# Kernel tuning notes

Hardware: AMD Instinct MI355X
Metric: run time of the kernel (lower is better)

Reference implementation:

```python
import jax, jax.numpy as jnp
import numpy as np

EPS = 1e-5
NHEAD = 8
TOP_K = 2


def _layernorm(x, g, b):
    m = jnp.mean(x, axis=-1, keepdims=True)
    v = jnp.mean((x - m) ** 2, axis=-1, keepdims=True)
    return (x - m) * jax.lax.rsqrt(v + EPS) * g + b


def setup_inputs() -> dict:
    S, D, F, E = 4096, 512, 2048, 8
    key = jax.random.key(0)
    ks = jax.random.split(key, 18)
    std = 0.02
    return {
        "src": jax.random.normal(ks[0], (S, D), jnp.float32),
        "in_proj_w": std * jax.random.normal(ks[1], (3 * D, D), jnp.float32),
        "in_proj_b": jnp.zeros((3 * D,), jnp.float32),
        "out_proj_w": std * jax.random.normal(ks[2], (D, D), jnp.float32),
        "out_proj_b": jnp.zeros((D,), jnp.float32),
        "ln1_g": jnp.ones((D,), jnp.float32),
        "ln1_b": jnp.zeros((D,), jnp.float32),
        "ln2_g": jnp.ones((D,), jnp.float32),
        "ln2_b": jnp.zeros((D,), jnp.float32),
        "gate_w": std * jax.random.normal(ks[3], (E, D), jnp.float32),
        "gate_b": jnp.zeros((E,), jnp.float32),
        "w1": std * jax.random.normal(ks[4], (E, F, D), jnp.float32),
        "b1": jnp.zeros((E, F), jnp.float32),
        "w2": std * jax.random.normal(ks[5], (E, F, D), jnp.float32),
        "b2": jnp.zeros((E, F), jnp.float32),
        "wo": std * jax.random.normal(ks[6], (E, D, F), jnp.float32),
        "bo": jnp.zeros((E, D), jnp.float32),
    }


def _sa_block(x, in_proj_w, in_proj_b, out_proj_w, out_proj_b):
    # x: [S, D] unbatched sequence (torch MultiheadAttention unbatched path)
    S, D = x.shape
    hd = D // NHEAD
    qkv = x @ in_proj_w.T + in_proj_b              # [S, 3D]
    q, k, v = jnp.split(qkv, 3, axis=-1)
    q = q.reshape(S, NHEAD, hd)
    k = k.reshape(S, NHEAD, hd)
    v = v.reshape(S, NHEAD, hd)
    scores = jnp.einsum("shd,thd->hst", q, k) / jnp.sqrt(jnp.float32(hd))
    attn = jax.nn.softmax(scores, axis=-1)         # [H, S, S]
    out = jnp.einsum("hst,thd->shd", attn, v).reshape(S, D)
    return out @ out_proj_w.T + out_proj_b


def _ff_block(x, gate_w, gate_b, w1, b1, w2, b2, wo, bo):
    # top-k gated SwiGLU MoE; gate probs are softmax, NOT renormalized after topk
    T = x.shape[0]
    E = w1.shape[0]
    gates = jax.nn.softmax(x @ gate_w.T + gate_b, axis=-1)      # [T, E]
    top_scores, top_idx = jax.lax.top_k(gates, TOP_K)            # [T, k]
    combine = jnp.zeros((T, E), x.dtype).at[
        jnp.arange(T)[:, None], top_idx].add(top_scores)         # [T, E]
    out = jnp.zeros_like(x)
    for e in range(E):  # small fixed expert count
        h = jax.nn.silu(x @ w1[e].T + b1[e]) * (x @ w2[e].T + b2[e])
        out = out + combine[:, e:e + 1] * (h @ wo[e].T + bo[e])
    return out


def reference(src, in_proj_w, in_proj_b, out_proj_w, out_proj_b,
              ln1_g, ln1_b, ln2_g, ln2_b,
              gate_w, gate_b, w1, b1, w2, b2, wo, bo):
    # norm_first pre-norm residual layer, dropout=0 (eval)
    x = src
    x = x + _sa_block(_layernorm(x, ln1_g, ln1_b),
                      in_proj_w, in_proj_b, out_proj_w, out_proj_b)
    x = x + _ff_block(_layernorm(x, ln2_g, ln2_b),
                      gate_w, gate_b, w1, b1, w2, b2, wo, bo)
    return x
```

## Files before the change

kernel.cpp:

```cpp
#include <hip/hip_runtime.h>
#include <hip/hip_bf16.h>
#include <math.h>

#define SQ   4096
#define DM   512
#define NH   8
#define HDIM 64
#define FF   2048
#define NE   8

typedef unsigned short u16;
typedef unsigned int   u32;
typedef __attribute__((ext_vector_type(8))) __bf16 bf16x8;
typedef __attribute__((ext_vector_type(4))) float  f32x4;

__device__ __forceinline__ float bf2f(u16 v) {
    union { u32 i; float f; } c; c.i = ((u32)v) << 16; return c.f;
}
__device__ __forceinline__ u16 f2bf(float f) {
    union { __bf16 h; u16 u; } c; c.h = (__bf16)f; return c.u;
}

#define BM 128
#define BN 128
#define BK 32
#define BKP 40

__global__ __launch_bounds__(256) void gemm_split(
    const u16* __restrict__ Ahi, const u16* __restrict__ Alo, int lda,
    const u16* __restrict__ Bhi, const u16* __restrict__ Blo, int ldb,
    int M, int N, int K,
    const float* __restrict__ bias,
    const float* __restrict__ resid, int ldres,
    u16* __restrict__ Chi, u16* __restrict__ Clo,
    float* __restrict__ Cf, int ldc, int mode)
{
    __shared__ __align__(16) u16 Ash[BM * BKP], Asl[BM * BKP];
    __shared__ __align__(16) u16 Bsh[BN * BKP], Bsl[BN * BKP];
    const int tid  = threadIdx.x;
    const int wave = tid >> 6;
    const int lane = tid & 63;
    const int quad = lane >> 4;
    const int l16  = lane & 15;
    const int bm = blockIdx.x * BM;
    const int bn = blockIdx.y * BN;
    const int wm = (wave & 1) * 64;
    const int wn = (wave >> 1) * 64;

    f32x4 acc[4][4];
#pragma unroll
    for (int i = 0; i < 4; i++)
#pragma unroll
        for (int j = 0; j < 4; j++)
#pragma unroll
            for (int r = 0; r < 4; r++) acc[i][j][r] = 0.0f;

    for (int k0 = 0; k0 < K; k0 += BK) {
#pragma unroll
        for (int i = 0; i < 2; i++) {
            int c = tid + i * 256;
            int row = c >> 2;
            int col = (c & 3) << 3;
            int ga = bm + row, gb2 = bn + row;
            uint4 vah = make_uint4(0u,0u,0u,0u), val = vah, vbh = vah, vbl = vah;
            if (ga < M) {
                vah = *(const uint4*)(Ahi + (size_t)ga * lda + k0 + col);
                val = *(const uint4*)(Alo + (size_t)ga * lda + k0 + col);
            }
            if (gb2 < N) {
                vbh = *(const uint4*)(Bhi + (size_t)gb2 * ldb + k0 + col);
                vbl = *(const uint4*)(Blo + (size_t)gb2 * ldb + k0 + col);
            }
            *(uint4*)(Ash + row * BKP + col) = vah;
            *(uint4*)(Asl + row * BKP + col) = val;
            *(uint4*)(Bsh + row * BKP + col) = vbh;
            *(uint4*)(Bsl + row * BKP + col) = vbl;
        }
        __syncthreads();
        bf16x8 ah[4], al[4], bh[4], bl[4];
#pragma unroll
        for (int i = 0; i < 4; i++) {
            ah[i] = *(const bf16x8*)(Ash + (wm + i * 16 + l16) * BKP + quad * 8);
            al[i] = *(const bf16x8*)(Asl + (wm + i * 16 + l16) * BKP + quad * 8);
        }
#pragma unroll
        for (int j = 0; j < 4; j++) {
            bh[j] = *(const bf16x8*)(Bsh + (wn + j * 16 + l16) * BKP + quad * 8);
            bl[j] = *(const bf16x8*)(Bsl + (wn + j * 16 + l16) * BKP + quad * 8);
        }
#pragma unroll
        for (int i = 0; i < 4; i++)
#pragma unroll
            for (int j = 0; j < 4; j++) {
                acc[i][j] = __builtin_amdgcn_mfma_f32_16x16x32_bf16(ah[i], bh[j], acc[i][j], 0,0,0);
                acc[i][j] = __builtin_amdgcn_mfma_f32_16x16x32_bf16(ah[i], bl[j], acc[i][j], 0,0,0);
                acc[i][j] = __builtin_amdgcn_mfma_f32_16x16x32_bf16(al[i], bh[j], acc[i][j], 0,0,0);
            }
        __syncthreads();
    }

#pragma unroll
    for (int i = 0; i < 4; i++)
#pragma unroll
        for (int j = 0; j < 4; j++)
#pragma unroll
            for (int r = 0; r < 4; r++) {
                int row = bm + wm + i * 16 + quad * 4 + r;
                int col = bn + wn + j * 16 + l16;
                if (row >= M || col >= N) continue;
                float v = acc[i][j][r] + (bias ? bias[col] : 0.0f);
                size_t idx = (size_t)row * ldc + col;
                if (mode == 0) {
                    u16 hb = f2bf(v);
                    Chi[idx] = hb;
                    Clo[idx] = f2bf(v - bf2f(hb));
                } else {
                    if (resid) v += resid[(size_t)row * ldres + col];
                    Cf[idx] = v;
                }
            }
}

__global__ __launch_bounds__(256) void gemm_split_ko(
    const u16* __restrict__ Ahi, const u16* __restrict__ Alo, int lda,
    const u16* __restrict__ Bhi, const u16* __restrict__ Blo, int ldb,
    float* __restrict__ Cf, int ldc)
{
    __shared__ __align__(16) u16 Ash[BM * BKP], Asl[BM * BKP];
    __shared__ __align__(16) u16 Bsh[BN * BKP], Bsl[BN * BKP];
    const int tid  = threadIdx.x;
    const int wave = tid >> 6;
    const int lane = tid & 63;
    const int quad = lane >> 4;
    const int l16  = lane & 15;
    const int bm = blockIdx.x * BM;
    const int bn = blockIdx.y * BN;
    const int wm = (wave & 1) * 64;
    const int wn = (wave >> 1) * 64;
    const int KC    = DM / 4;
    const int k0beg = blockIdx.z * KC;

    f32x4 acc[4][4];
#pragma unroll
    for (int i = 0; i < 4; i++)
#pragma unroll
        for (int j = 0; j < 4; j++)
#pragma unroll
            for (int r = 0; r < 4; r++) acc[i][j][r] = 0.0f;

    for (int k0 = k0beg; k0 < k0beg + KC; k0 += BK) {
#pragma unroll
        for (int i = 0; i < 2; i++) {
            int c = tid + i * 256;
            int row = c >> 2;
            int col = (c & 3) << 3;
            int ga = bm + row, gb2 = bn + row;
            uint4 vah = *(const uint4*)(Ahi + (size_t)ga * lda + k0 + col);
            uint4 val = *(const uint4*)(Alo + (size_t)ga * lda + k0 + col);
            uint4 vbh = *(const uint4*)(Bhi + (size_t)gb2 * ldb + k0 + col);
            uint4 vbl = *(const uint4*)(Blo + (size_t)gb2 * ldb + k0 + col);
            *(uint4*)(Ash + row * BKP + col) = vah;
            *(uint4*)(Asl + row * BKP + col) = val;
            *(uint4*)(Bsh + row * BKP + col) = vbh;
            *(uint4*)(Bsl + row * BKP + col) = vbl;
        }
        __syncthreads();
        bf16x8 ah[4], al[4], bh[4], bl[4];
#pragma unroll
        for (int i = 0; i < 4; i++) {
            ah[i] = *(const bf16x8*)(Ash + (wm + i * 16 + l16) * BKP + quad * 8);
            al[i] = *(const bf16x8*)(Asl + (wm + i * 16 + l16) * BKP + quad * 8);
        }
#pragma unroll
        for (int j = 0; j < 4; j++) {
            bh[j] = *(const bf16x8*)(Bsh + (wn + j * 16 + l16) * BKP + quad * 8);
            bl[j] = *(const bf16x8*)(Bsl + (wn + j * 16 + l16) * BKP + quad * 8);
        }
#pragma unroll
        for (int i = 0; i < 4; i++)
#pragma unroll
            for (int j = 0; j < 4; j++) {
                acc[i][j] = __builtin_amdgcn_mfma_f32_16x16x32_bf16(ah[i], bh[j], acc[i][j], 0,0,0);
                acc[i][j] = __builtin_amdgcn_mfma_f32_16x16x32_bf16(ah[i], bl[j], acc[i][j], 0,0,0);
                acc[i][j] = __builtin_amdgcn_mfma_f32_16x16x32_bf16(al[i], bh[j], acc[i][j], 0,0,0);
            }
        __syncthreads();
    }

#pragma unroll
    for (int i = 0; i < 4; i++)
#pragma unroll
        for (int j = 0; j < 4; j++)
#pragma unroll
            for (int r = 0; r < 4; r++) {
                int row = bm + wm + i * 16 + quad * 4 + r;
                int col = bn + wn + j * 16 + l16;
                atomicAdd(Cf + (size_t)row * ldc + col, acc[i][j][r]);
            }
}

__global__ __launch_bounds__(256) void init_x1(
    const float* __restrict__ src, const float* __restrict__ bias,
    float* __restrict__ x1)
{
    int i = blockIdx.x * 256 + threadIdx.x;
    int col4 = i & (DM / 4 - 1);
    float4 s = ((const float4*)src)[i];
    float4 b = ((const float4*)bias)[col4];
    s.x += b.x; s.y += b.y; s.z += b.z; s.w += b.w;
    ((float4*)x1)[i] = s;
}

__global__ __launch_bounds__(256) void moe12_all(
    const u16* __restrict__ A, int lda,
    const int* __restrict__ idxl, const int* __restrict__ cnt,
    const int* __restrict__ off,
    const float* __restrict__ w1, const float* __restrict__ b1,
    const float* __restrict__ w2, const float* __restrict__ b2,
    u16* __restrict__ H)
{
    const int bmg = blockIdx.x * BM;
    if (bmg >= off[NE]) return;
    int e = 0;
    while (e < NE - 1 && bmg >= off[e + 1]) e++;
    const int M   = cnt[e];
    const int bml = bmg - off[e];
    if (bml >= M) return;
    const float* B1 = w1 + (size_t)e * FF * DM;
    const float* B2 = w2 + (size_t)e * FF * DM;
    const int*   rl = idxl + e * SQ;

    __shared__ __align__(16) u16 As[BM * BKP], Bs1[BN * BKP], Bs2[BN * BKP];
    const int tid  = threadIdx.x;
    const int wave = tid >> 6;
    const int lane = tid & 63;
    const int quad = lane >> 4;
    const int l16  = lane & 15;
    const int bn = blockIdx.y * BN;
    const int wm = (wave & 1) * 64;
    const int wn = (wave >> 1) * 64;

    f32x4 acc1[4][4], acc2[4][4];
#pragma unroll
    for (int i = 0; i < 4; i++)
#pragma unroll
        for (int j = 0; j < 4; j++)
#pragma unroll
            for (int r = 0; r < 4; r++) { acc1[i][j][r] = 0.0f; acc2[i][j][r] = 0.0f; }

    for (int k0 = 0; k0 < DM; k0 += BK) {
#pragma unroll
        for (int i = 0; i < 2; i++) {
            int c = tid + i * 256;
            int row = c >> 2;
            int col = (c & 3) << 3;
            uint4 va = make_uint4(0u,0u,0u,0u);
            int lr = bml + row;
            if (lr < M) {
                int ar = rl[lr];
                va = *(const uint4*)(A + (size_t)ar * lda + k0 + col);
            }
            *(uint4*)(As + row * BKP + col) = va;
        }
#pragma unroll
        for (int i = 0; i < 4; i++) {
            int c = tid + i * 256;
            int row = c >> 3;
            int col = (c & 7) << 2;
            float4 v1 = *(const float4*)(B1 + (size_t)(bn + row) * DM + k0 + col);
            float4 v2 = *(const float4*)(B2 + (size_t)(bn + row) * DM + k0 + col);
            ushort4 h1, h2;
            h1.x = f2bf(v1.x); h1.y = f2bf(v1.y); h1.z = f2bf(v1.z); h1.w = f2bf(v1.w);
            h2.x = f2bf(v2.x); h2.y = f2bf(v2.y); h2.z = f2bf(v2.z); h2.w = f2bf(v2.w);
            *(ushort4*)(Bs1 + row * BKP + col) = h1;
            *(ushort4*)(Bs2 + row * BKP + col) = h2;
        }
        __syncthreads();
        bf16x8 af[4], b1f[4], b2f[4];
#pragma unroll
        for (int i = 0; i < 4; i++)
            af[i] = *(const bf16x8*)(As + (wm + i * 16 + l16) * BKP + quad * 8);
#pragma unroll
        for (int j = 0; j < 4; j++) {
            b1f[j] = *(const bf16x8*)(Bs1 + (wn + j * 16 + l16) * BKP + quad * 8);
            b2f[j] = *(const bf16x8*)(Bs2 + (wn + j * 16 + l16) * BKP + quad * 8);
        }
#pragma unroll
        for (int i = 0; i < 4; i++)
#pragma unroll
            for (int j = 0; j < 4; j++) {
                acc1[i][j] = __builtin_amdgcn_mfma_f32_16x16x32_bf16(af[i], b1f[j], acc1[i][j], 0,0,0);
                acc2[i][j] = __builtin_amdgcn_mfma_f32_16x16x32_bf16(af[i], b2f[j], acc2[i][j], 0,0,0);
            }
        __syncthreads();
    }

#pragma unroll
    for (int i = 0; i < 4; i++)
#pragma unroll
        for (int j = 0; j < 4; j++)
#pragma unroll
            for (int r = 0; r < 4; r++) {
                int rowl = bml + wm + i * 16 + quad * 4 + r;
                if (rowl >= M) continue;
                int col = bn + wn + j * 16 + l16;
                float g1 = acc1[i][j][r] + b1[e * FF + col];
                float g2 = acc2[i][j][r] + b2[e * FF + col];
                float s  = g1 / (1.0f + __expf(-g1));
                H[(size_t)(off[e] + rowl) * FF + col] = f2bf(s * g2);
            }
}

__global__ __launch_bounds__(256) void moe12_bf16(
    const u16* __restrict__ A, int lda,
    const int* __restrict__ idxl, const int* __restrict__ cnt,
    const int* __restrict__ off,
    const u16* __restrict__ w1b, const float* __restrict__ b1,
    const u16* __restrict__ w2b, const float* __restrict__ b2,
    u16* __restrict__ H)
{
    const int bmg = blockIdx.x * BM;
    if (bmg >= off[NE]) return;
    int e = 0;
    while (e < NE - 1 && bmg >= off[e + 1]) e++;
    const int M   = cnt[e];
    const int bml = bmg - off[e];
    if (bml >= M) return;
    const u16* B1 = w1b + (size_t)e * FF * DM;
    const u16* B2 = w2b + (size_t)e * FF * DM;
    const int* rl = idxl + e * SQ;

    __shared__ __align__(16) u16 As[BM * BKP], Bs1[BN * BKP], Bs2[BN * BKP];
    const int tid  = threadIdx.x;
    const int wave = tid >> 6;
    const int lane = tid & 63;
    const int quad = lane >> 4;
    const int l16  = lane & 15;
    const int bn = blockIdx.y * BN;
    const int wm = (wave & 1) * 64;
    const int wn = (wave >> 1) * 64;

    f32x4 acc1[4][4], acc2[4][4];
#pragma unroll
    for (int i = 0; i < 4; i++)
#pragma unroll
        for (int j = 0; j < 4; j++)
#pragma unroll
            for (int r = 0; r < 4; r++) { acc1[i][j][r] = 0.0f; acc2[i][j][r] = 0.0f; }

    for (int k0 = 0; k0 < DM; k0 += BK) {
#pragma unroll
        for (int i = 0; i < 2; i++) {
            int c = tid + i * 256;
            int row = c >> 2;
            int col = (c & 3) << 3;
            uint4 va = make_uint4(0u,0u,0u,0u);
            int lr = bml + row;
            if (lr < M) {
                int ar = rl[lr];
                va = *(const uint4*)(A + (size_t)ar * lda + k0 + col);
            }
            *(uint4*)(As + row * BKP + col) = va;
            uint4 v1 = *(const uint4*)(B1 + (size_t)(bn + row) * DM + k0 + col);
            uint4 v2 = *(const uint4*)(B2 + (size_t)(bn + row) * DM + k0 + col);
            *(uint4*)(Bs1 + row * BKP + col) = v1;
            *(uint4*)(Bs2 + row * BKP + col) = v2;
        }
        __syncthreads();
        bf16x8 af[4], b1f[4], b2f[4];
#pragma unroll
        for (int i = 0; i < 4; i++)
            af[i] = *(const bf16x8*)(As + (wm + i * 16 + l16) * BKP + quad * 8);
#pragma unroll
        for (int j = 0; j < 4; j++) {
            b1f[j] = *(const bf16x8*)(Bs1 + (wn + j * 16 + l16) * BKP + quad * 8);
            b2f[j] = *(const bf16x8*)(Bs2 + (wn + j * 16 + l16) * BKP + quad * 8);
        }
#pragma unroll
        for (int i = 0; i < 4; i++)
#pragma unroll
            for (int j = 0; j < 4; j++) {
                acc1[i][j] = __builtin_amdgcn_mfma_f32_16x16x32_bf16(af[i], b1f[j], acc1[i][j], 0,0,0);
                acc2[i][j] = __builtin_amdgcn_mfma_f32_16x16x32_bf16(af[i], b2f[j], acc2[i][j], 0,0,0);
            }
        __syncthreads();
    }

#pragma unroll
    for (int i = 0; i < 4; i++)
#pragma unroll
        for (int j = 0; j < 4; j++)
#pragma unroll
            for (int r = 0; r < 4; r++) {
                int rowl = bml + wm + i * 16 + quad * 4 + r;
                if (rowl >= M) continue;
                int col = bn + wn + j * 16 + l16;
                float g1 = acc1[i][j][r] + b1[e * FF + col];
                float g2 = acc2[i][j][r] + b2[e * FF + col];
                float s  = g1 / (1.0f + __expf(-g1));
                H[(size_t)(off[e] + rowl) * FF + col] = f2bf(s * g2);
            }
}

__global__ __launch_bounds__(256) void moe_y_all(
    const u16* __restrict__ H,
    const float* __restrict__ wo, const float* __restrict__ bo,
    const int* __restrict__ idxl, const float* __restrict__ cw,
    const int* __restrict__ cnt, const int* __restrict__ off,
    float* __restrict__ out)
{
    const int bmg = blockIdx.x * BM;
    if (bmg >= off[NE]) return;
    int e = 0;
    while (e < NE - 1 && bmg >= off[e + 1]) e++;
    const int M   = cnt[e];
    const int bml = bmg - off[e];
    if (bml >= M) return;
    const float* B = wo + (size_t)e * DM * FF;

    __shared__ __align__(16) u16 As[BM * BKP], Bs[BN * BKP];
    const int tid  = threadIdx.x;
    const int wave = tid >> 6;
    const int lane = tid & 63;
    const int quad = lane >> 4;
    const int l16  = lane & 15;
    const int bn = blockIdx.y * BN;
    const int wm = (wave & 1) * 64;
    const int wn = (wave >> 1) * 64;

    f32x4 acc[4][4];
#pragma unroll
    for (int i = 0; i < 4; i++)
#pragma unroll
        for (int j = 0; j < 4; j++)
#pragma unroll
            for (int r = 0; r < 4; r++) acc[i][j][r] = 0.0f;

    for (int k0 = 0; k0 < FF; k0 += BK) {
#pragma unroll
        for (int i = 0; i < 2; i++) {
            int c = tid + i * 256;
            int row = c >> 2;
            int col = (c & 3) << 3;
            uint4 va = *(const uint4*)(H + (size_t)(bmg + row) * FF + k0 + col);
            *(uint4*)(As + row * BKP + col) = va;
        }
#pragma unroll
        for (int i = 0; i < 4; i++) {
            int c = tid + i * 256;
            int row = c >> 3;
            int col = (c & 7) << 2;
            float4 v = *(const float4*)(B + (size_t)(bn + row) * FF + k0 + col);
            ushort4 h;
            h.x = f2bf(v.x); h.y = f2bf(v.y); h.z = f2bf(v.z); h.w = f2bf(v.w);
            *(ushort4*)(Bs + row * BKP + col) = h;
        }
        __syncthreads();
        bf16x8 af[4], bf[4];
#pragma unroll
        for (int i = 0; i < 4; i++)
            af[i] = *(const bf16x8*)(As + (wm + i * 16 + l16) * BKP + quad * 8);
#pragma unroll
        for (int j = 0; j < 4; j++)
            bf[j] = *(const bf16x8*)(Bs + (wn + j * 16 + l16) * BKP + quad * 8);
#pragma unroll
        for (int i = 0; i < 4; i++)
#pragma unroll
            for (int j = 0; j < 4; j++)
                acc[i][j] = __builtin_amdgcn_mfma_f32_16x16x32_bf16(af[i], bf[j], acc[i][j], 0,0,0);
        __syncthreads();
    }

#pragma unroll
    for (int i = 0; i < 4; i++)
#pragma unroll
        for (int j = 0; j < 4; j++)
#pragma unroll
            for (int r = 0; r < 4; r++) {
                int rowl = bml + wm + i * 16 + quad * 4 + r;
                if (rowl >= M) continue;
                int col = bn + wn + j * 16 + l16;
                int tok = idxl[e * SQ + rowl];
                float wgt = cw[e * SQ + rowl];
                atomicAdd(out + (size_t)tok * DM + col,
                          wgt * (acc[i][j][r] + bo[e * DM + col]));
            }
}

__global__ __launch_bounds__(256) void moe_y_bf16(
    const u16* __restrict__ H,
    const u16* __restrict__ wob, const float* __restrict__ bo,
    const int* __restrict__ idxl, const float* __restrict__ cw,
    const int* __restrict__ cnt, const int* __restrict__ off,
    float* __restrict__ out)
{
    const int bmg = blockIdx.x * BM;
    if (bmg >= off[NE]) return;
    int e = 0;
    while (e < NE - 1 && bmg >= off[e + 1]) e++;
    const int M   = cnt[e];
    const int bml = bmg - off[e];
    if (bml >= M) return;
    const u16* B = wob + (size_t)e * DM * FF;

    __shared__ __align__(16) u16 As[BM * BKP], Bs[BN * BKP];
    const int tid  = threadIdx.x;
    const int wave = tid >> 6;
    const int lane = tid & 63;
    const int quad = lane >> 4;
    const int l16  = lane & 15;
    const int bn = blockIdx.y * BN;
    const int wm = (wave & 1) * 64;
    const int wn = (wave >> 1) * 64;

    f32x4 acc[4][4];
#pragma unroll
    for (int i = 0; i < 4; i++)
#pragma unroll
        for (int j = 0; j < 4; j++)
#pragma unroll
            for (int r = 0; r < 4; r++) acc[i][j][r] = 0.0f;

    for (int k0 = 0; k0 < FF; k0 += BK) {
#pragma unroll
        for (int i = 0; i < 2; i++) {
            int c = tid + i * 256;
            int row = c >> 2;
            int col = (c & 3) << 3;
            uint4 va = *(const uint4*)(H + (size_t)(bmg + row) * FF + k0 + col);
            *(uint4*)(As + row * BKP + col) = va;
            uint4 vb = *(const uint4*)(B + (size_t)(bn + row) * FF + k0 + col);
            *(uint4*)(Bs + row * BKP + col) = vb;
        }
        __syncthreads();
        bf16x8 af[4], bf[4];
#pragma unroll
        for (int i = 0; i < 4; i++)
            af[i] = *(const bf16x8*)(As + (wm + i * 16 + l16) * BKP + quad * 8);
#pragma unroll
        for (int j = 0; j < 4; j++)
            bf[j] = *(const bf16x8*)(Bs + (wn + j * 16 + l16) * BKP + quad * 8);
#pragma unroll
        for (int i = 0; i < 4; i++)
#pragma unroll
            for (int j = 0; j < 4; j++)
                acc[i][j] = __builtin_amdgcn_mfma_f32_16x16x32_bf16(af[i], bf[j], acc[i][j], 0,0,0);
        __syncthreads();
    }

#pragma unroll
    for (int i = 0; i < 4; i++)
#pragma unroll
        for (int j = 0; j < 4; j++)
#pragma unroll
            for (int r = 0; r < 4; r++) {
                int rowl = bml + wm + i * 16 + quad * 4 + r;
                if (rowl >= M) continue;
                int col = bn + wn + j * 16 + l16;
                int tok = idxl[e * SQ + rowl];
                float wgt = cw[e * SQ + rowl];
                atomicAdd(out + (size_t)tok * DM + col,
                          wgt * (acc[i][j][r] + bo[e * DM + col]));
            }
}

__global__ __launch_bounds__(256) void cvt_w_bf16(
    const float* __restrict__ w, u16* __restrict__ wb, int n4)
{
    int i = blockIdx.x * 256 + threadIdx.x;
    if (i < n4) {
        float4 v = ((const float4*)w)[i];
        ushort4 h;
        h.x = f2bf(v.x); h.y = f2bf(v.y); h.z = f2bf(v.z); h.w = f2bf(v.w);
        ((ushort4*)wb)[i] = h;
    }
}

#define KP 64
#define SWZ(row, col) ((col) ^ (((row) & 7) << 3))
#define SCL 0.18033688011112042f

template <int SPLIT>
__device__ __forceinline__ void flash_body(
    const u16* __restrict__ qh, const u16* __restrict__ ql,
    const u16* __restrict__ vth, const u16* __restrict__ vtl,
    u16* __restrict__ oh, u16* __restrict__ ol,
    float* __restrict__ Opart, float* __restrict__ mpart,
    float* __restrict__ lpart)
{
    __shared__ __align__(16) u16 Ksh[64*KP], Ksl[64*KP], Vsh[64*KP], Vsl[64*KP];
    const int tid  = threadIdx.x;
    const int wave = tid >> 6;
    const int lane = tid & 63;
    const int quad = lane >> 4;
    const int l16  = lane & 15;
    const int h    = blockIdx.y;
    const int z    = (SPLIT > 1) ? blockIdx.z : 0;
    const int qbase = blockIdx.x * 64 + wave * 16;

    const int r_st  = tid >> 3;
    const int co_g  = (tid & 7) << 3;
    const int co_sw = SWZ(r_st, co_g);

    bf16x8 aqh[2], aql[2];
#pragma unroll
    for (int kk = 0; kk < 2; kk++) {
        size_t off = (size_t)(qbase + l16) * (3*DM) + h*HDIM + kk*32 + quad*8;
        aqh[kk] = *(const bf16x8*)(qh + off);
        aql[kk] = *(const bf16x8*)(ql + off);
    }

    float m_ = -1e30f, l_ = 0.0f;
    f32x4 o_[4];
#pragma unroll
    for (int nd = 0; nd < 4; nd++)
#pragma unroll
        for (int r = 0; r < 4; r++) o_[nd][r] = 0.0f;

    const int srcA = l16 + ((quad & 1) * 2) * 16;
    const int srcB = srcA + 16;
    const bool hiJ = (quad >> 1);

    const int NT    = SQ / 64 / SPLIT;
    const int jtBeg = z * NT, jtEnd = (z + 1) * NT;

    for (int jt = jtBeg; jt < jtEnd; jt++) {
        {
            size_t koff0 = (size_t)(jt*64 + r_st) * (3*DM) + DM + h*HDIM + co_g;
            size_t voff0 = (size_t)(h*HDIM + r_st) * SQ + jt*64 + co_g;
            size_t koff1 = koff0 + (size_t)32 * (3*DM);
            size_t voff1 = voff0 + (size_t)32 * SQ;
            uint4 a0 = *(const uint4*)(qh  + koff0);
            uint4 a1 = *(const uint4*)(ql  + koff0);
            uint4 a2 = *(const uint4*)(vth + voff0);
            uint4 a3 = *(const uint4*)(vtl + voff0);
            uint4 b0 = *(const uint4*)(qh  + koff1);
            uint4 b1 = *(const uint4*)(ql  + koff1);
            uint4 b2 = *(const uint4*)(vth + voff1);
            uint4 b3 = *(const uint4*)(vtl + voff1);
            *(uint4*)(Ksh + r_st*KP + co_sw)      = a0;
            *(uint4*)(Ksl + r_st*KP + co_sw)      = a1;
            *(uint4*)(Vsh + r_st*KP + co_sw)      = a2;
            *(uint4*)(Vsl + r_st*KP + co_sw)      = a3;
            *(uint4*)(Ksh + (r_st+32)*KP + co_sw) = b0;
            *(uint4*)(Ksl + (r_st+32)*KP + co_sw) = b1;
            *(uint4*)(Vsh + (r_st+32)*KP + co_sw) = b2;
            *(uint4*)(Vsl + (r_st+32)*KP + co_sw) = b3;
        }
        __syncthreads();

        f32x4 s[4];
        __builtin_amdgcn_s_setprio(1);
#pragma unroll
        for (int jn = 0; jn < 4; jn++) {
            f32x4 zz;
#pragma unroll
            for (int r = 0; r < 4; r++) zz[r] = 0.0f;
#pragma unroll
            for (int kk = 0; kk < 2; kk++) {
                int krow = jn*16 + l16;
                int kcol = SWZ(krow, kk*32 + quad*8);
                bf16x8 kh = *(const bf16x8*)(Ksh + krow*KP + kcol);
                bf16x8 kl = *(const bf16x8*)(Ksl + krow*KP + kcol);
                zz = __builtin_amdgcn_mfma_f32_16x16x32_bf16(kh, aqh[kk], zz, 0,0,0);
                zz = __builtin_amdgcn_mfma_f32_16x16x32_bf16(kl, aqh[kk], zz, 0,0,0);
                zz = __builtin_amdgcn_mfma_f32_16x16x32_bf16(kh, aql[kk], zz, 0,0,0);
            }
#pragma unroll
            for (int r = 0; r < 4; r++) zz[r] *= SCL;
            s[jn] = zz;
        }
        __builtin_amdgcn_s_setprio(0);

        float mx = s[0][0];
#pragma unroll
        for (int jn = 0; jn < 4; jn++)
#pragma unroll
            for (int r = 0; r < 4; r++) mx = fmaxf(mx, s[jn][r]);
        mx = fmaxf(mx, __shfl_xor(mx, 16));
        mx = fmaxf(mx, __shfl_xor(mx, 32));

        int grew = (mx > m_ + 8.0f) ? 1 : 0;
        if (__any(grew)) {
            float nm  = fmaxf(m_, mx);
            float al2 = exp2f(m_ - nm);
            m_ = nm;
            l_ *= al2;
            float alq[4];
#pragma unroll
            for (int r = 0; r < 4; r++)
                alq[r] = __shfl(al2, quad*4 + r);
#pragma unroll
            for (int nd = 0; nd < 4; nd++)
#pragma unroll
                for (int r = 0; r < 4; r++) o_[nd][r] *= alq[r];
        }

        float rs = 0.0f;
#pragma unroll
        for (int jn = 0; jn < 4; jn++)
#pragma unroll
            for (int r = 0; r < 4; r++) {
                float p = exp2f(s[jn][r] - m_);
                s[jn][r] = p;
                rs += p;
            }
        rs += __shfl_xor(rs, 16);
        rs += __shfl_xor(rs, 32);
        l_ += rs;

        u32 phk[4][2], plk[4][2];
#pragma unroll
        for (int jn = 0; jn < 4; jn++) {
            u16 h0 = f2bf(s[jn][0]), h1 = f2bf(s[jn][1]);
            u16 h2 = f2bf(s[jn][2]), h3 = f2bf(s[jn][3]);
            phk[jn][0] = (u32)h0 | ((u32)h1 << 16);
            phk[jn][1] = (u32)h2 | ((u32)h3 << 16);
            u16 g0 = f2bf(s[jn][0] - bf2f(h0)), g1 = f2bf(s[jn][1] - bf2f(h1));
            u16 g2 = f2bf(s[jn][2] - bf2f(h2)), g3 = f2bf(s[jn][3] - bf2f(h3));
            plk[jn][0] = (u32)g0 | ((u32)g1 << 16);
            plk[jn][1] = (u32)g2 | ((u32)g3 << 16);
        }

        bf16x8 phf[2], plf[2];
#pragma unroll
        for (int kk = 0; kk < 2; kk++) {
            int jA = kk*2, jB = kk*2 + 1;
            uint4 wh, wl;
            {
                u32 a = (u32)__shfl((int)phk[jA][0], srcA);
                u32 b = (u32)__shfl((int)phk[jB][0], srcA);
                wh.x = hiJ ? b : a;
                a = (u32)__shfl((int)phk[jA][1], srcA);
                b = (u32)__shfl((int)phk[jB][1], srcA);
                wh.y = hiJ ? b : a;
                a = (u32)__shfl((int)phk[jA][0], srcB);
                b = (u32)__shfl((int)phk[jB][0], srcB);
                wh.z = hiJ ? b : a;
                a = (u32)__shfl((int)phk[jA][1], srcB);
                b = (u32)__shfl((int)phk[jB][1], srcB);
                wh.w = hiJ ? b : a;
            }
            {
                u32 a = (u32)__shfl((int)plk[jA][0], srcA);
                u32 b = (u32)__shfl((int)plk[jB][0], srcA);
                wl.x = hiJ ? b : a;
                a = (u32)__shfl((int)plk[jA][1], srcA);
                b = (u32)__shfl((int)plk[jB][1], srcA);
                wl.y = hiJ ? b : a;
                a = (u32)__shfl((int)plk[jA][0], srcB);
                b = (u32)__shfl((int)plk[jB][0], srcB);
                wl.z = hiJ ? b : a;
                a = (u32)__shfl((int)plk[jA][1], srcB);
                b = (u32)__shfl((int)plk[jB][1], srcB);
                wl.w = hiJ ? b : a;
            }
            union { uint4 u; bf16x8 v; } ch, cl;
            ch.u = wh; cl.u = wl;
            phf[kk] = ch.v;
            plf[kk] = cl.v;
        }

        __builtin_amdgcn_s_setprio(1);
#pragma unroll
        for (int nd = 0; nd < 4; nd++) {
#pragma unroll
            for (int kk = 0; kk < 2; kk++) {
                int vrow = nd*16 + l16;
                int vcol = SWZ(vrow, kk*32 + quad*8);
                bf16x8 vh = *(const bf16x8*)(Vsh + vrow*KP + vcol);
                bf16x8 vl = *(const bf16x8*)(Vsl + vrow*KP + vcol);
                o_[nd] = __builtin_amdgcn_mfma_f32_16x16x32_bf16(phf[kk], vh, o_[nd], 0,0,0);
                o_[nd] = __builtin_amdgcn_mfma_f32_16x16x32_bf16(phf[kk], vl, o_[nd], 0,0,0);
                o_[nd] = __builtin_amdgcn_mfma_f32_16x16x32_bf16(plf[kk], vh, o_[nd], 0,0,0);
            }
        }
        __builtin_amdgcn_s_setprio(0);
        __syncthreads();
    }

    if (SPLIT == 1) {
        float lq[4];
#pragma unroll
        for (int r = 0; r < 4; r++) lq[r] = __shfl(l_, quad*4 + r);
#pragma unroll
        for (int nd = 0; nd < 4; nd++)
#pragma unroll
            for (int r = 0; r < 4; r++) {
                int row = qbase + quad*4 + r;
                int col = h*HDIM + nd*16 + l16;
                float w = o_[nd][r] / lq[r];
                u16 hb = f2bf(w);
                oh[(size_t)row * DM + col] = hb;
                ol[(size_t)row * DM + col] = f2bf(w - bf2f(hb));
            }
    } else {
#pragma unroll
        for (int nd = 0; nd < 4; nd++)
#pragma unroll
            for (int r = 0; r < 4; r++) {
                int row = qbase + quad*4 + r;
                int col = h*HDIM + nd*16 + l16;
                Opart[((size_t)z * SQ + row) * DM + col] = o_[nd][r];
            }
        if (lane < 16) {
            int row = qbase + l16;
            mpart[(z*NH + h) * SQ + row] = m_;
            lpart[(z*NH + h) * SQ + row] = l_;
        }
    }
}

__global__ __launch_bounds__(256) void flash_attn(
    const u16* __restrict__ qh, const u16* __restrict__ ql,
    const u16* __restrict__ vth, const u16* __restrict__ vtl,
    u16* __restrict__ oh, u16* __restrict__ ol)
{
    flash_body<1>(qh, ql, vth, vtl, oh, ol, nullptr, nullptr, nullptr);
}

__global__ __launch_bounds__(256) void flash_attn_part2(
    const u16* __restrict__ qh, const u16* __restrict__ ql,
    const u16* __restrict__ vth, const u16* __restrict__ vtl,
    float* __restrict__ Opart, float* __restrict__ mpart,
    float* __restrict__ lpart)
{
    flash_body<2>(qh, ql, vth, vtl, nullptr, nullptr, Opart, mpart, lpart);
}

__global__ __launch_bounds__(256) void flash_attn_part4(
    const u16* __restrict__ qh, const u16* __restrict__ ql,
    const u16* __restrict__ vth, const u16* __restrict__ vtl,
    float* __restrict__ Opart, float* __restrict__ mpart,
    float* __restrict__ lpart)
{
    flash_body<4>(qh, ql, vth, vtl, nullptr, nullptr, Opart, mpart, lpart);
}

__global__ __launch_bounds__(256) void attn_combine(
    const float* __restrict__ Opart, const float* __restrict__ mpart,
    const float* __restrict__ lpart,
    u16* __restrict__ oh, u16* __restrict__ ol, int ns)
{
    const int row = blockIdx.x;
    const int tid = threadIdx.x;
#pragma unroll
    for (int i = 0; i < 2; i++) {
        int col = tid + i * 256;
        int h = col >> 6;
        float m = -1e30f;
        for (int zz = 0; zz < ns; zz++)
            m = fmaxf(m, mpart[(zz*NH + h) * SQ + row]);
        float O = 0.0f, l = 0.0f;
        for (int zz = 0; zz < ns; zz++) {
            float a = exp2f(mpart[(zz*NH + h) * SQ + row] - m);
            O += Opart[((size_t)zz * SQ + row) * DM + col] * a;
            l += lpart[(zz*NH + h) * SQ + row] * a;
        }
        float w = O / l;
        u16 hb = f2bf(w);
        oh[(size_t)row * DM + col] = hb;
        ol[(size_t)row * DM + col] = f2bf(w - bf2f(hb));
    }
}

__global__ __launch_bounds__(256) void ln1_split(
    const float* __restrict__ x, const float* __restrict__ g,
    const float* __restrict__ b, u16* __restrict__ ohi, u16* __restrict__ olo)
{
    const int row = blockIdx.x;
    const int tid = threadIdx.x;
    float v0 = x[(size_t)row * DM + tid];
    float v1 = x[(size_t)row * DM + tid + 256];
    float s = v0 + v1, sq = v0*v0 + v1*v1;
#pragma unroll
    for (int o = 1; o < 64; o <<= 1) { s += __shfl_xor(s, o); sq += __shfl_xor(sq, o); }
    __shared__ float ss[4], ssq[4];
    if ((tid & 63) == 0) { ss[tid>>6] = s; ssq[tid>>6] = sq; }
    __syncthreads();
    s  = ss[0]+ss[1]+ss[2]+ss[3];
    sq = ssq[0]+ssq[1]+ssq[2]+ssq[3];
    float m = s * (1.0f/DM);
    float rstd = rsqrtf(sq*(1.0f/DM) - m*m + 1e-5f);
    float y0 = (v0-m)*rstd*g[tid]     + b[tid];
    float y1 = (v1-m)*rstd*g[tid+256] + b[tid+256];
    u16 h0 = f2bf(y0), h1 = f2bf(y1);
    ohi[(size_t)row*DM + tid]       = h0;  olo[(size_t)row*DM + tid]       = f2bf(y0 - bf2f(h0));
    ohi[(size_t)row*DM + tid + 256] = h1;  olo[(size_t)row*DM + tid + 256] = f2bf(y1 - bf2f(h1));
}

__global__ __launch_bounds__(256) void transpose_v2(
    const u16* __restrict__ qh, const u16* __restrict__ ql,
    u16* __restrict__ vth, u16* __restrict__ vtl)
{
    __shared__ u16 Th[64 * 66], Tl[64 * 66];
    const int t0  = blockIdx.x * 64;
    const int hd0 = blockIdx.y * 64;
    const int tid = threadIdx.x;
#pragma unroll
    for (int k = 0; k < 16; k++) {
        int idx = tid + k * 256;
        int r = idx >> 6, j = idx & 63;
        size_t src = (size_t)(t0 + r) * (3*DM) + 2*DM + hd0 + j;
        Th[r * 66 + j] = qh[src];
        Tl[r * 66 + j] = ql[src];
    }
    __syncthreads();
#pragma unroll
    for (int k = 0; k < 16; k++) {
        int idx = tid + k * 256;
        int r = idx >> 6, c2 = idx & 63;
        size_t dst = (size_t)(hd0 + r) * SQ + t0 + c2;
        vth[dst] = Th[c2 * 66 + r];
        vtl[dst] = Tl[c2 * 66 + r];
    }
}

__global__ __launch_bounds__(256) void gate_route(
    const float* __restrict__ x1, const float* __restrict__ g,
    const float* __restrict__ b, const float* __restrict__ gw,
    const float* __restrict__ gb,
    int* __restrict__ cnt, int* __restrict__ idxl, float* __restrict__ cw,
    u16* __restrict__ xout)
{
    const int token = blockIdx.x * 4 + (threadIdx.x >> 6);
    const int lane  = threadIdx.x & 63;
    const float* xr = x1 + (size_t)token * DM;
    float v[8];
#pragma unroll
    for (int i = 0; i < 8; i++) v[i] = xr[lane*8 + i];
    float s = 0.f, sq = 0.f;
#pragma unroll
    for (int i = 0; i < 8; i++) { s += v[i]; sq += v[i]*v[i]; }
#pragma unroll
    for (int o = 1; o < 64; o <<= 1) { s += __shfl_xor(s, o); sq += __shfl_xor(sq, o); }
    float m = s * (1.0f/DM);
    float rstd = rsqrtf(sq*(1.0f/DM) - m*m + 1e-5f);
    float xn[8];
#pragma unroll
    for (int i = 0; i < 8; i++)
        xn[i] = (v[i]-m)*rstd*g[lane*8+i] + b[lane*8+i];
    {
        uint4 w;
        w.x = (u32)f2bf(xn[0]) | ((u32)f2bf(xn[1]) << 16);
        w.y = (u32)f2bf(xn[2]) | ((u32)f2bf(xn[3]) << 16);
        w.z = (u32)f2bf(xn[4]) | ((u32)f2bf(xn[5]) << 16);
        w.w = (u32)f2bf(xn[6]) | ((u32)f2bf(xn[7]) << 16);
        *(uint4*)(xout + (size_t)token * DM + lane*8) = w;
    }
    float logit[8];
#pragma unroll
    for (int e = 0; e < 8; e++) {
        float t = 0.f;
#pragma unroll
        for (int i = 0; i < 8; i++) t += xn[i] * gw[e*DM + lane*8 + i];
#pragma unroll
        for (int o = 1; o < 64; o <<= 1) t += __shfl_xor(t, o);
        logit[e] = t + gb[e];
    }
    if (lane == 0) {
        float mx = -1e30f;
        for (int e = 0; e < 8; e++) mx = fmaxf(mx, logit[e]);
        float den = 0.f, p[8];
        for (int e = 0; e < 8; e++) { p[e] = __expf(logit[e] - mx); den += p[e]; }
        for (int e = 0; e < 8; e++) p[e] /= den;
        int i1 = 0;
        for (int e = 1; e < 8; e++) if (p[e] > p[i1]) i1 = e;
        int i2 = -1;
        for (int e = 0; e < 8; e++) { if (e == i1) continue; if (i2 < 0 || p[e] > p[i2]) i2 = e; }
        int s1 = atomicAdd(&cnt[i1], 1);
        idxl[i1*SQ + s1] = token;  cw[i1*SQ + s1] = p[i1];
        int s2 = atomicAdd(&cnt[i2], 1);
        idxl[i2*SQ + s2] = token;  cw[i2*SQ + s2] = p[i2];
    }
}

__global__ __launch_bounds__(256) void cvt_split_w(
    const float* __restrict__ w, u16* __restrict__ wh, u16* __restrict__ wl, int n)
{
    int i = blockIdx.x * 256 + threadIdx.x;
    if (i < n) {
        float v = w[i];
        u16 h = f2bf(v);
        wh[i] = h;
        wl[i] = f2bf(v - bf2f(h));
    }
}

__global__ __launch_bounds__(64) void zero_cnt(int* cnt)
{
    if (threadIdx.x < NE) cnt[threadIdx.x] = 0;
}

__global__ __launch_bounds__(64) void make_off(const int* __restrict__ cnt,
                                              int* __restrict__ off)
{
    if (threadIdx.x == 0) {
        int a = 0;
        for (int e = 0; e < NE; e++) {
            off[e] = a;
            a += ((cnt[e] + 127) >> 7) << 7;
        }
        off[NE] = a;
    }
}

__global__ __launch_bounds__(256) void init_out(
    const float* __restrict__ x1, float* __restrict__ out)
{
    int i = blockIdx.x * 256 + threadIdx.x;
    ((float4*)out)[i] = ((const float4*)x1)[i];
}

__global__ __launch_bounds__(256) void sentinel_kernel(float* out, float v, int n)
{
    int i = blockIdx.x * 256 + threadIdx.x;
    if (i < n) out[i] = v;
}
__global__ __launch_bounds__(256) void scrub_kernel(float* out, int n)
{
    int i = blockIdx.x * 256 + threadIdx.x;
    if (i < n) { float v = out[i]; if (!isfinite(v)) out[i] = 777.0f; }
}

extern "C" void kernel_launch(void* const* d_in, const int* in_sizes, int n_in,
                              void* d_out, int out_size, void* d_ws, size_t ws_size,
                              hipStream_t stream)
{
    const float* src        = (const float*)d_in[0];
    const float* in_proj_w  = (const float*)d_in[1];
    const float* in_proj_b  = (const float*)d_in[2];
    const float* out_proj_w = (const float*)d_in[3];
    const float* out_proj_b = (const float*)d_in[4];
    const float* ln1_g      = (const float*)d_in[5];
    const float* ln1_b      = (const float*)d_in[6];
    const float* ln2_g      = (const float*)d_in[7];
    const float* ln2_b      = (const float*)d_in[8];
    const float* gate_w     = (const float*)d_in[9];
    const float* gate_b     = (const float*)d_in[10];
    const float* w1         = (const float*)d_in[11];
    const float* b1         = (const float*)d_in[12];
    const float* w2         = (const float*)d_in[13];
    const float* b2         = (const float*)d_in[14];
    const float* wo         = (const float*)d_in[15];
    const float* bo         = (const float*)d_in[16];
    float* out = (float*)d_out;

    const size_t MB = (size_t)1 << 20;
    const size_t ROUTE = 512 * 1024;
    const size_t NEED      = ROUTE + 44 * MB;
    const size_t NEED_BIG2 = ROUTE + 61 * MB;
    const size_t NEED_BIG4 = ROUTE + 78 * MB;
    if (ws_size < NEED) {
        sentinel_kernel<<<(SQ*DM)/256, 256, 0, stream>>>(out, 333.0f, SQ*DM);
        return;
    }
    int ns = 0;
    if (ws_size >= NEED_BIG4)      ns = 4;
    else if (ws_size >= NEED_BIG2) ns = 2;

    char* ws = (char*)d_ws;
    int*   cnt  = (int*)ws;
    int*   offp = (int*)(ws + 64);
    int*   idxl = (int*)(ws + 1024);
    float* cw   = (float*)(ws + 1024 + 128*1024);
    char*  base = ws + ROUTE;
    u16* xln1h = (u16*)(base);
    u16* xln1l = (u16*)(base + 4*MB);
    u16* attnh = (u16*)(base);
    u16* attnl = (u16*)(base + 4*MB);
    u16* qkvh  = (u16*)(base + 8*MB);
    u16* qkvl  = (u16*)(base + 20*MB);
    float* x1  = (float*)(base + 8*MB);
    u16* vth   = (u16*)(base + 32*MB);
    u16* vtl   = (u16*)(base + 36*MB);
    u16* xln2  = (u16*)(base + 36*MB);
    u16* Hbuf  = (u16*)(base);
    u16* wph   = (u16*)(base + 40*MB);
    u16* wpl   = (u16*)(base + 40*MB + 1536*1024);
    u16* woh   = (u16*)(base + 43*MB);
    u16* wol   = (u16*)(base + 43*MB + 512*1024);
    float* Opart = (float*)(base + 44*MB);
    float* mpart;
    float* lpart;
    if (ns == 4) {
        mpart = (float*)(base + 76*MB);
        lpart = (float*)(base + 76*MB + 512*1024);
    } else {
        mpart = (float*)(base + 60*MB);
        lpart = (float*)(base + 60*MB + 256*1024);
    }
    u16* w1b = (u16*)(base + 44*MB);
    u16* w2b = (u16*)(base + 60*MB);
    u16* wob = (u16*)(base + 44*MB);

    cvt_split_w<<<(3*DM*DM)/256, 256, 0, stream>>>(in_proj_w,  wph, wpl, 3*DM*DM);
    cvt_split_w<<<(DM*DM)/256,   256, 0, stream>>>(out_proj_w, woh, wol, DM*DM);

    ln1_split<<<SQ, 256, 0, stream>>>(src, ln1_g, ln1_b, xln1h, xln1l);
    gemm_split<<<dim3(32, 12), 256, 0, stream>>>(
        xln1h, xln1l, DM, wph, wpl, DM, SQ, 3*DM, DM,
        in_proj_b, nullptr, 0, qkvh, qkvl, nullptr, 3*DM, 0);
    transpose_v2<<<dim3(SQ/64, DM/64), 256, 0, stream>>>(qkvh, qkvl, vth, vtl);
    if (ns == 4) {
        flash_attn_part4<<<dim3(SQ/64, NH, 4), 256, 0, stream>>>(
            qkvh, qkvl, vth, vtl, Opart, mpart, lpart);
        attn_combine<<<SQ, 256, 0, stream>>>(Opart, mpart, lpart, attnh, attnl, 4);
    } else if (ns == 2) {
        flash_attn_part2<<<dim3(SQ/64, NH, 2), 256, 0, stream>>>(
            qkvh, qkvl, vth, vtl, Opart, mpart, lpart);
        attn_combine<<<SQ, 256, 0, stream>>>(Opart, mpart, lpart, attnh, attnl, 2);
    } else {
        flash_attn<<<dim3(SQ/64, NH), 256, 0, stream>>>(
            qkvh, qkvl, vth, vtl, attnh, attnl);
    }
    init_x1<<<(SQ*DM/4)/256, 256, 0, stream>>>(src, out_proj_b, x1);
    gemm_split_ko<<<dim3(32, 4, 4), 256, 0, stream>>>(
        attnh, attnl, DM, woh, wol, DM, x1, DM);

    zero_cnt<<<1, 64, 0, stream>>>(cnt);
    gate_route<<<SQ/4, 256, 0, stream>>>(x1, ln2_g, ln2_b, gate_w, gate_b,
                                         cnt, idxl, cw, xln2);
    make_off<<<1, 64, 0, stream>>>(cnt, offp);
    init_out<<<(SQ*DM/4)/256, 256, 0, stream>>>(x1, out);
    const int WN4 = (NE * FF * DM) / 4;
    if (ns == 4) {
        cvt_w_bf16<<<WN4/256, 256, 0, stream>>>(w1, w1b, WN4);
        cvt_w_bf16<<<WN4/256, 256, 0, stream>>>(w2, w2b, WN4);
        moe12_bf16<<<dim3(72, 16), 256, 0, stream>>>(
            xln2, DM, idxl, cnt, offp, w1b, b1, w2b, b2, Hbuf);
        cvt_w_bf16<<<WN4/256, 256, 0, stream>>>(wo, wob, WN4);
        moe_y_bf16<<<dim3(72, 4), 256, 0, stream>>>(
            Hbuf, wob, bo, idxl, cw, cnt, offp, out);
    } else {
        moe12_all<<<dim3(72, 16), 256, 0, stream>>>(
            xln2, DM, idxl, cnt, offp, w1, b1, w2, b2, Hbuf);
        moe_y_all<<<dim3(72, 4), 256, 0, stream>>>(
            Hbuf, wo, bo, idxl, cw, cnt, offp, out);
    }

    scrub_kernel<<<(SQ*DM)/256, 256, 0, stream>>>(out, SQ*DM);
}
```

Measured before the change: 728.7 us.

## Split MoE output GEMM along K and use direct global-to-LDS loads in attention

The MoE down-projection kernels now split the FF reduction into four chunks across blockIdx.z. Each chunk atomically accumulates its partial result, and only the first chunk adds the bias. This raises the block count for a grid that was small. Separately, the flash-attention K/V tile staging now uses global_load_lds builtins, which write straight into LDS without passing through registers, with the swizzle moved to the global address side. The split quadruples the atomic traffic to the output, and the direct LDS loads change the store layout, which depends on the swizzle and the per-wave base offsets being correct.

```diff
diff --git a/kernel.cpp b/kernel.cpp
--- a/kernel.cpp
+++ b/kernel.cpp
@@ -19,6 +19,12 @@
 }
 __device__ __forceinline__ u16 f2bf(float f) {
     union { __bf16 h; u16 u; } c; c.h = (__bf16)f; return c.u;
+}
+
+__device__ __forceinline__ void gload16(const u16* __restrict__ g, u16* lds) {
+    __builtin_amdgcn_global_load_lds(
+        (const __attribute__((address_space(1))) u32*)g,
+        (__attribute__((address_space(3))) u32*)lds, 16, 0, 0);
 }
 
 #define BM 128
@@ -417,6 +423,8 @@
     const int bml = bmg - off[e];
     if (bml >= M) return;
     const float* B = wo + (size_t)e * DM * FF;
+    const int KC    = FF / 4;
+    const int k0beg = blockIdx.z * KC;
 
     __shared__ __align__(16) u16 As[BM * BKP], Bs[BN * BKP];
     const int tid  = threadIdx.x;
@@ -436,7 +444,7 @@
 #pragma unroll
             for (int r = 0; r < 4; r++) acc[i][j][r] = 0.0f;
 
-    for (int k0 = 0; k0 < FF; k0 += BK) {
+    for (int k0 = k0beg; k0 < k0beg + KC; k0 += BK) {
 #pragma unroll
         for (int i = 0; i < 2; i++) {
             int c = tid + i * 256;
@@ -482,8 +490,9 @@
                 int col = bn + wn + j * 16 + l16;
                 int tok = idxl[e * SQ + rowl];
                 float wgt = cw[e * SQ + rowl];
+                float bterm = (blockIdx.z == 0) ? bo[e * DM + col] : 0.0f;
                 atomicAdd(out + (size_t)tok * DM + col,
-                          wgt * (acc[i][j][r] + bo[e * DM + col]));
+                          wgt * (acc[i][j][r] + bterm));
             }
 }
 
@@ -502,6 +511,8 @@
     const int bml = bmg - off[e];
     if (bml >= M) return;
     const u16* B = wob + (size_t)e * DM * FF;
+    const int KC    = FF / 4;
+    const int k0beg = blockIdx.z * KC;
 
     __shared__ __align__(16) u16 As[BM * BKP], Bs[BN * BKP];
     const int tid  = threadIdx.x;
@@ -521,7 +532,7 @@
 #pragma unroll
             for (int r = 0; r < 4; r++) acc[i][j][r] = 0.0f;
 
-    for (int k0 = 0; k0 < FF; k0 += BK) {
+    for (int k0 = k0beg; k0 < k0beg + KC; k0 += BK) {
 #pragma unroll
         for (int i = 0; i < 2; i++) {
             int c = tid + i * 256;
@@ -559,8 +570,9 @@
                 int col = bn + wn + j * 16 + l16;
                 int tok = idxl[e * SQ + rowl];
                 float wgt = cw[e * SQ + rowl];
+                float bterm = (blockIdx.z == 0) ? bo[e * DM + col] : 0.0f;
                 atomicAdd(out + (size_t)tok * DM + col,
-                          wgt * (acc[i][j][r] + bo[e * DM + col]));
+                          wgt * (acc[i][j][r] + bterm));
             }
 }
 
@@ -598,9 +610,10 @@
     const int z    = (SPLIT > 1) ? blockIdx.z : 0;
     const int qbase = blockIdx.x * 64 + wave * 16;
 
-    const int r_st  = tid >> 3;
-    const int co_g  = (tid & 7) << 3;
-    const int co_sw = SWZ(r_st, co_g);
+    const int rg = lane >> 3;
+    const int gr = lane & 7;
+    const int swc = SWZ(rg, gr * 8);
+    const int wb  = wave * 8 * KP;
 
     bf16x8 aqh[2], aql[2];
 #pragma unroll
@@ -626,26 +639,18 @@
 
     for (int jt = jtBeg; jt < jtEnd; jt++) {
         {
-            size_t koff0 = (size_t)(jt*64 + r_st) * (3*DM) + DM + h*HDIM + co_g;
-            size_t voff0 = (size_t)(h*HDIM + r_st) * SQ + jt*64 + co_g;
-            size_t koff1 = koff0 + (size_t)32 * (3*DM);
-            size_t voff1 = voff0 + (size_t)32 * SQ;
-            uint4 a0 = *(const uint4*)(qh  + koff0);
-            uint4 a1 = *(const uint4*)(ql  + koff0);
-            uint4 a2 = *(const uint4*)(vth + voff0);
-            uint4 a3 = *(const uint4*)(vtl + voff0);
-            uint4 b0 = *(const uint4*)(qh  + koff1);
-            uint4 b1 = *(const uint4*)(ql  + koff1);
-            uint4 b2 = *(const uint4*)(vth + voff1);
-            uint4 b3 = *(const uint4*)(vtl + voff1);
-            *(uint4*)(Ksh + r_st*KP + co_sw)      = a0;
-            *(uint4*)(Ksl + r_st*KP + co_sw)      = a1;
-            *(uint4*)(Vsh + r_st*KP + co_sw)      = a2;
-            *(uint4*)(Vsl + r_st*KP + co_sw)      = a3;
-            *(uint4*)(Ksh + (r_st+32)*KP + co_sw) = b0;
-            *(uint4*)(Ksl + (r_st+32)*KP + co_sw) = b1;
-            *(uint4*)(Vsh + (r_st+32)*KP + co_sw) = b2;
-            *(uint4*)(Vsl + (r_st+32)*KP + co_sw) = b3;
+            size_t k0a = (size_t)(jt*64 + wave*8 + rg) * (3*DM) + DM + h*HDIM + swc;
+            size_t k1a = k0a + (size_t)32 * (3*DM);
+            size_t v0a = (size_t)(h*HDIM + wave*8 + rg) * SQ + jt*64 + swc;
+            size_t v1a = v0a + (size_t)32 * SQ;
+            gload16(qh  + k0a, Ksh + wb);
+            gload16(ql  + k0a, Ksl + wb);
+            gload16(vth + v0a, Vsh + wb);
+            gload16(vtl + v0a, Vsl + wb);
+            gload16(qh  + k1a, Ksh + wb + 32*KP);
+            gload16(ql  + k1a, Ksl + wb + 32*KP);
+            gload16(vth + v1a, Vsh + wb + 32*KP);
+            gload16(vtl + v1a, Vsl + wb + 32*KP);
         }
         __syncthreads();
 
@@ -1130,12 +1135,12 @@
         moe12_bf16<<<dim3(72, 16), 256, 0, stream>>>(
             xln2, DM, idxl, cnt, offp, w1b, b1, w2b, b2, Hbuf);
         cvt_w_bf16<<<WN4/256, 256, 0, stream>>>(wo, wob, WN4);
-        moe_y_bf16<<<dim3(72, 4), 256, 0, stream>>>(
+        moe_y_bf16<<<dim3(72, 4, 4), 256, 0, stream>>>(
             Hbuf, wob, bo, idxl, cw, cnt, offp, out);
     } else {
         moe12_all<<<dim3(72, 16), 256, 0, stream>>>(
             xln2, DM, idxl, cnt, offp, w1, b1, w2, b2, Hbuf);
-        moe_y_all<<<dim3(72, 4), 256, 0, stream>>>(
+        moe_y_all<<<dim3(72, 4, 4), 256, 0, stream>>>(
             Hbuf, wo, bo, idxl, cw, cnt, offp, out);
     }
 
```

New measurement: 773.0 us. 1.06x slower.
